# Performance work log

Measured on AMD Instinct MI355X. Metric: run time of the kernel, lower is better.

## Reference

```python
import jax, jax.numpy as jnp
import numpy as np

KSIZE, STRIDE, SCALE = 7, 4, 10.0


def _same_pad_amounts(n, k, s):
    out = -(-n // s)
    pad = max(0, (out - 1) * s + k - n)
    return pad // 2, pad - pad // 2, out


def _conv(x, w, b, stride=1, pad=0):
    y = jax.lax.conv_general_dilated(
        x, w, (stride, stride), [(pad, pad), (pad, pad)],
        dimension_numbers=("NCHW", "OIHW", "NCHW"))
    return y + b[None, :, None, None]


def setup_inputs() -> dict:
    key = jax.random.key(0)
    ks = jax.random.split(key, 10)
    B, Cin, H, W = 2, 64, 256, 256
    Ci = 16                       # inter_channels
    d_in = KSIZE * KSIZE * Ci     # 784 = ksize^2 * inter_channels
    d_out = d_in // 4             # 196
    s = 0.02
    return {
        "b": jax.random.normal(ks[0], (B, Cin, H, W), jnp.float32),
        "g_w": jax.random.normal(ks[1], (Ci, Cin, 3, 3), jnp.float32) * s,
        "g_b": jnp.zeros((Ci,), jnp.float32),
        "theta_w": jax.random.normal(ks[2], (Ci, Cin, 1, 1), jnp.float32) * s,
        "theta_b": jnp.zeros((Ci,), jnp.float32),
        "W_w": jax.random.normal(ks[3], (Cin, Ci, 1, 1), jnp.float32) * s,
        "W_b": jnp.zeros((Cin,), jnp.float32),
        "fc1_w": jax.random.normal(ks[4], (d_out, d_in), jnp.float32) * s,
        "fc1_b": jnp.zeros((d_out,), jnp.float32),
        "fc2_w": jax.random.normal(ks[5], (d_out, d_in), jnp.float32) * s,
        "fc2_b": jnp.zeros((d_out,), jnp.float32),
        "thr_w": jax.random.normal(ks[6], (1, Cin, KSIZE, KSIZE), jnp.float32) * s,
        "thr_b": jnp.zeros((1,), jnp.float32),
        "bias_w": jax.random.normal(ks[7], (1, Cin, KSIZE, KSIZE), jnp.float32) * s,
        "bias_b": jnp.zeros((1,), jnp.float32),
    }


def _forward(b, g_w, g_b, theta_w, theta_b, W_w, W_b, fc1_w, fc1_b,
             fc2_w, fc2_b, thr_w, thr_b, bias_w, bias_b):
    B, Cin, H, W = b.shape
    k, s = KSIZE, STRIDE
    pt, pb, Lh = _same_pad_amounts(H, k, s)
    pl, pr, Lw = _same_pad_amounts(W, k, s)
    L = Lh * Lw
    Ci = g_w.shape[0]

    b1 = _conv(b, g_w, g_b, 1, 1)            # [B,Ci,H,W]
    b2 = _conv(b, theta_w, theta_b, 1, 0)    # [B,Ci,H,W]
    b4 = jnp.pad(b, ((0, 0), (0, 0), (pt, pb), (pl, pr)))
    thr = _conv(b4, thr_w, thr_b, s, 0).reshape(B, L)   # per-patch threshold
    bias = _conv(b4, bias_w, bias_b, s, 0).reshape(B, L)  # per-patch bias

    # patch gather indices on the 'same'-padded grid (torch.Unfold order)
    R = (jnp.arange(Lh) * s)[:, None] + jnp.arange(k)[None, :]   # [Lh,k]
    Cc = (jnp.arange(Lw) * s)[:, None] + jnp.arange(k)[None, :]  # [Lw,k]
    Ri = R[:, None, :, None]                                     # -> [Lh,Lw,k,k]
    Cj = Cc[None, :, None, :]

    def patches(x):  # [B,Ci,H,W] -> [B,L,Ci*k*k], flatten order (C,kh,kw)
        xp = jnp.pad(x, ((0, 0), (0, 0), (pt, pb), (pl, pr)))
        p = xp[:, :, Ri, Cj]                       # [B,Ci,Lh,Lw,k,k]
        return p.transpose(0, 2, 3, 1, 4, 5).reshape(B, L, -1)

    wi = patches(b1)     # stride_1 patches of b1
    xi = wi              # b3 = b1 and stride_1 == stride_2 -> identical patches
    pi = patches(b2)     # stride_2 patches of b2, values to aggregate

    wi_f = jax.nn.relu(jnp.einsum("bld,od->blo", wi, fc1_w) + fc1_b)
    xi_f = jax.nn.relu(jnp.einsum("bld,od->blo", xi, fc2_w) + fc2_b)
    score = jnp.einsum("blo,bmo->blm", wi_f, xi_f)   # [B,L,L] patch similarity

    # threshold-gated sparse attention with learned per-patch thr/bias
    mask = (score >= thr[:, :, None]).astype(score.dtype)
    gated = score * mask + bias[:, :, None]
    attn = jax.nn.softmax(gated * SCALE, axis=-1) * mask
    attn = attn / (attn.sum(-1, keepdims=True) + 1e-8)

    agg = jnp.einsum("blm,bmd->bld", attn, pi)       # [B,L,Ci*k*k]
    p6 = agg.reshape(B, Lh, Lw, Ci, k, k).transpose(0, 3, 1, 2, 4, 5)

    # fold back (sum overlaps), normalize by overlap count, crop padding
    Hp, Wp = H + pt + pb, W + pl + pr
    folded = jnp.zeros((B, Ci, Hp, Wp), score.dtype).at[:, :, Ri, Cj].add(p6)
    cnt = jnp.zeros((Hp, Wp), score.dtype).at[Ri, Cj].add(1.0)
    zi = (folded / cnt)[:, :, pl:pl + H, pt:pt + W]

    return b + _conv(zi, W_w, W_b, 1, 0)


def reference(b, g_w, g_b, theta_w, theta_b, W_w, W_b, fc1_w, fc1_b,
              fc2_w, fc2_b, thr_w, thr_b, bias_w, bias_b):
    return _forward(b, g_w, g_b, theta_w, theta_b, W_w, W_b, fc1_w, fc1_b,
                    fc2_w, fc2_b, thr_w, thr_b, bias_w, bias_b)
```

## Files before the change

kernel.cpp:

```cpp
#include <hip/hip_runtime.h>
#include <math.h>

#define CIN  64
#define CI   16
#define HH   256
#define WWD  256
#define KS   7
#define STR  4
#define LH   64
#define LWD  64
#define LL   4096
#define DIN  784
#define DINP 896
#define DKP  832
#define DOUT 196
#define DOUTP 256
#define NB   2
#define YP   258
#define XP   264

typedef __attribute__((ext_vector_type(8))) short bf16x8;
typedef __attribute__((ext_vector_type(4))) float f32x4;
typedef __attribute__((ext_vector_type(16))) float f32x16;
typedef __attribute__((ext_vector_type(8))) int i32x8;
typedef __attribute__((ext_vector_type(4))) int i32x4;

__device__ __forceinline__ unsigned short f2bf(float x) {
    unsigned int u = __float_as_uint(x);
    unsigned int r = (u + 0x7FFFu + ((u >> 16) & 1u)) >> 16;
    return (unsigned short)r;
}
__device__ __forceinline__ float bf2f(unsigned short h) {
    return __uint_as_float(((unsigned int)h) << 16);
}

__device__ __forceinline__ void stage16(const void* g, void* l) {
#if defined(__has_builtin)
#if __has_builtin(__builtin_amdgcn_global_load_lds)
    __builtin_amdgcn_global_load_lds(
        (const __attribute__((address_space(1))) unsigned int*)g,
        (__attribute__((address_space(3))) unsigned int*)l, 16, 0, 0);
    return;
#endif
#endif
    *(float4*)l = *(const float4*)g;
}

__global__ __launch_bounds__(256) void k_prep_b(const float* __restrict__ b,
                                                unsigned short* __restrict__ bTp) {
    int blk = blockIdx.x;
    int s = blk & 7; int yy = (blk >> 3) % YP; int n = blk / (8 * YP);
    int y = yy - 1;
    for (int xx = threadIdx.x; xx < XP; xx += 256) {
        int x = xx - 4;
        bool v = (y >= 0 && y < 256 && x >= 0 && x < 256);
        unsigned short h[8];
#pragma unroll
        for (int j = 0; j < 8; j++)
            h[j] = v ? f2bf(b[((size_t)(n * 64 + s * 8 + j) * 256 + y) * 256 + x]) : (unsigned short)0;
        *(uint4*)&bTp[((((size_t)n * YP + yy) * 8 + s) * XP + xx) * 8] = *(uint4*)h;
    }
}

__global__ void k_prep_wb(const float* __restrict__ g_w, const float* __restrict__ th_w,
                          unsigned short* __restrict__ wbt) {
    int i = blockIdx.x * 256 + threadIdx.x;
    if (i >= 18432) return;
    int j = i & 7, co = (i >> 3) & 31, q = (i >> 8) & 3, h = (i >> 10) & 1, t = i >> 11;
    int ci = h * 32 + q * 8 + j;
    float v;
    if (co < 16) v = g_w[((size_t)co * 64 + ci) * 9 + t];
    else         v = (t == 4) ? th_w[(size_t)(co - 16) * 64 + ci] : 0.f;
    wbt[i] = f2bf(v);
}

__global__ void k_prep_fc(const float* __restrict__ fc1_w, const float* __restrict__ fc2_w,
                          unsigned short* __restrict__ fcwb) {
    int i = blockIdx.x * 256 + threadIdx.x;
    if (i >= 2 * DOUTP * DKP) return;
    int col = i % DKP; int row = (i / DKP) % DOUTP; int f = i / (DKP * DOUTP);
    float v = 0.f;
    if (row < DOUT && col < DIN) v = (f ? fc2_w : fc1_w)[row * DIN + col];
    fcwb[i] = f2bf(v);
}

__global__ __launch_bounds__(256) void k_convm(
        const unsigned short* __restrict__ bTp, const unsigned short* __restrict__ wbt,
        const float* __restrict__ g_b, const float* __restrict__ th_b,
        unsigned short* __restrict__ bx) {
    __shared__ unsigned short wb[18432];
    __shared__ unsigned short ti[8 * 3 * 68 * 8];
    int tid = threadIdx.x;
#pragma unroll
    for (int i = 0; i < 9; i++) {
        int c = i * 256 + tid;
        stage16(wbt + (size_t)c * 8, &wb[c * 8]);
    }
    int n = blockIdx.x >> 8, y = blockIdx.x & 255;
    int wave = tid >> 6, lane = tid & 63, lr = lane & 15, q = lane >> 4;
    int m0 = wave * 16;
    float bg = g_b[lr], bt = th_b[lr];
    for (int xs = 0; xs < 4; xs++) {
        __syncthreads();
        int x0 = xs * 64;
#pragma unroll
        for (int i = 0; i < 7; i++) {
            int c = i * 256 + tid;
            if (c < 1632) {
                int s = c / 204; int rem = c % 204; int r = rem / 68; int cc = rem % 68;
                const unsigned short* src =
                    bTp + ((((size_t)n * YP + y + r) * 8 + s) * XP + (x0 + 3 + cc)) * 8;
                stage16(src, &ti[c * 8]);
            }
        }
        __syncthreads();
        f32x4 a0 = {bg, bg, bg, bg}, a1 = {bt, bt, bt, bt};
#pragma unroll
        for (int t = 0; t < 9; t++) {
            int dy = t / 3, dx = t % 3;
#pragma unroll
            for (int h = 0; h < 2; h++) {
                int s = h * 4 + q;
                bf16x8 av = *(const bf16x8*)&ti[(((s * 3 + dy) * 68) + m0 + lr + dx) * 8];
                bf16x8 b0 = *(const bf16x8*)&wb[((((t * 2 + h) * 4 + q) * 32) + lr) * 8];
                bf16x8 b1 = *(const bf16x8*)&wb[((((t * 2 + h) * 4 + q) * 32) + 16 + lr) * 8];
                a0 = __builtin_amdgcn_mfma_f32_16x16x32_bf16(av, b0, a0, 0, 0, 0);
                a1 = __builtin_amdgcn_mfma_f32_16x16x32_bf16(av, b1, a1, 0, 0, 0);
            }
        }
        size_t pb = (((size_t)n * 256 + y) * 256 + x0 + m0 + q * 4);
#pragma unroll
        for (int r = 0; r < 4; r++) {
            bx[(pb + r) * 32 + lr]      = f2bf(a0[r]);
            bx[(pb + r) * 32 + 16 + lr] = f2bf(a1[r]);
        }
    }
}

__global__ __launch_bounds__(256) void k_thr(
        const unsigned short* __restrict__ bTp, const float* __restrict__ thr_w,
        const float* __restrict__ thr_b, float* __restrict__ thr) {
    __shared__ float w[64 * 49];
    int tid = threadIdx.x;
    for (int i = tid; i < 64 * 49; i += 256) w[i] = thr_w[i];
    __syncthreads();
    int wid = (blockIdx.x << 2) + (tid >> 6);
    int lane = tid & 63;
    int s = lane >> 3, j = lane & 7;
    int n = wid >> 12, l = wid & 4095;
    int lh = (l >> 6), lw = l & 63;
    const float* wl = w + (s * 8 + j) * 49;
    float acc = 0.f;
#pragma unroll
    for (int dy = 0; dy < 7; dy++) {
        int yy = lh * 4 + dy;
        if (yy >= YP) continue;
        const unsigned short* row = bTp + (((size_t)(n * YP + yy) * 8 + s) * XP) * 8;
#pragma unroll
        for (int dx = 0; dx < 7; dx++) {
            int xx = lw * 4 + dx + 3;
            acc = fmaf(bf2f(row[xx * 8 + j]), wl[dy * 7 + dx], acc);
        }
    }
#pragma unroll
    for (int off = 32; off > 0; off >>= 1) acc += __shfl_down(acc, off, 64);
    if (lane == 0) thr[wid] = acc + thr_b[0];
}

__global__ void k_patchesA(const unsigned short* __restrict__ bx, unsigned short* __restrict__ Pb) {
    size_t e = (size_t)blockIdx.x * 256 + threadIdx.x;
    if (e >= (size_t)NB * LL * DKP) return;
    int d = (int)(e % DKP); size_t r = e / DKP;
    int l = (int)(r & 4095); int n = (int)(r >> 12);
    unsigned short v = 0;
    if (d < DIN) {
        int ci = d / 49; int t = d % 49; int dy = t / 7; int dx = t % 7;
        int y = (l >> 6) * 4 + dy - 1, x = (l & 63) * 4 + dx - 1;
        if (y >= 0 && y < 256 && x >= 0 && x < 256)
            v = bx[(((size_t)n * 256 + y) * 256 + x) * 32 + ci];
    }
    Pb[e] = v;
}

__global__ void k_patchesT(const unsigned short* __restrict__ bx, unsigned char* __restrict__ piT8) {
    size_t e = (size_t)blockIdx.x * 256 + threadIdx.x;
    int l = (int)(e & 4095);
    int d = (int)((e >> 12) % DINP);
    int n = (int)(e / ((size_t)DINP * LL));
    float v = 0.f;
    if (d < DIN) {
        int ci = d / 49; int t = d % 49; int dy = t / 7; int dx = t % 7;
        int y = (l >> 6) * 4 + dy - 1, x = (l & 63) * 4 + dx - 1;
        if (y >= 0 && y < 256 && x >= 0 && x < 256)
            v = bf2f(bx[(((size_t)n * 256 + y) * 256 + x) * 32 + 16 + ci]);
    }
    int p = __builtin_amdgcn_cvt_pk_fp8_f32(v, 0.f, 0, false);
    piT8[e] = (unsigned char)(p & 0xFF);
}

template<int MODE>
__global__ __launch_bounds__(256) void k_gemm_nt(
        const unsigned short* __restrict__ A, const unsigned short* __restrict__ Bt,
        void* __restrict__ C, int lda, int ldb, int ldc, int K,
        size_t sA, size_t sB, size_t sC,
        const float* __restrict__ bias1, const float* __restrict__ bias2) {
    __shared__ unsigned short lA[128 * 64];
    __shared__ unsigned short lB[128 * 64];
    int tid = threadIdx.x;
    int wave = tid >> 6, lane = tid & 63;
    int lr = lane & 15, lq = lane >> 4;
    int wm = (wave >> 1) * 64, wn = (wave & 1) * 64;
    int i0 = blockIdx.x * 128, j0 = blockIdx.y * 128;
    int z = blockIdx.z;
    int az = (MODE == 2) ? (z >> 1) : z;
    int bz = (MODE == 2) ? (z & 1) : z;
    const unsigned short* Ab = A + (size_t)az * sA + (size_t)i0 * lda;
    const unsigned short* Bb = Bt + (size_t)bz * sB + (size_t)j0 * ldb;
    f32x4 acc[4][4] = {};
    for (int k0 = 0; k0 < K; k0 += 64) {
        __syncthreads();
#pragma unroll
        for (int it = 0; it < 4; it++) {
            int c = it * 256 + tid;
            int row = c >> 3, slot = c & 7;
            int col8 = slot ^ (row & 7);
            stage16(Ab + (size_t)row * lda + k0 + col8 * 8, &lA[c * 8]);
        }
#pragma unroll
        for (int it = 0; it < 4; it++) {
            int c = it * 256 + tid;
            int row = c >> 3, slot = c & 7;
            int col8 = slot ^ (row & 7);
            stage16(Bb + (size_t)row * ldb + k0 + col8 * 8, &lB[c * 8]);
        }
        __syncthreads();
#pragma unroll
        for (int ks = 0; ks < 2; ks++) {
            bf16x8 af[4], bfr[4];
#pragma unroll
            for (int t = 0; t < 4; t++) {
                int row = wm + t * 16 + lr;
                int slot = ks * 4 + lq;
                af[t] = *(const bf16x8*)&lA[row * 64 + (slot ^ (row & 7)) * 8];
            }
#pragma unroll
            for (int t = 0; t < 4; t++) {
                int row = wn + t * 16 + lr;
                int slot = ks * 4 + lq;
                bfr[t] = *(const bf16x8*)&lB[row * 64 + (slot ^ (row & 7)) * 8];
            }
#pragma unroll
            for (int mi = 0; mi < 4; mi++)
#pragma unroll
                for (int nj = 0; nj < 4; nj++)
                    acc[mi][nj] = __builtin_amdgcn_mfma_f32_16x16x32_bf16(
                        af[mi], bfr[nj], acc[mi][nj], 0, 0, 0);
        }
    }
    if (MODE == 1) {
        unsigned short* Cb = (unsigned short*)C + (size_t)z * sC;
#pragma unroll
        for (int mi = 0; mi < 4; mi++)
#pragma unroll
            for (int r = 0; r < 4; r++) {
                int row = i0 + wm + mi * 16 + lq * 4 + r;
#pragma unroll
                for (int nj = 0; nj < 4; nj++)
                    Cb[(size_t)row * ldc + j0 + wn + nj * 16 + lr] = f2bf(acc[mi][nj][r]);
            }
    } else {
        const float* biasp = bz ? bias2 : bias1;
        unsigned short* Cb = (unsigned short*)C + (size_t)z * sC;
#pragma unroll
        for (int mi = 0; mi < 4; mi++)
#pragma unroll
            for (int r = 0; r < 4; r++) {
                int row = i0 + wm + mi * 16 + lq * 4 + r;
#pragma unroll
                for (int nj = 0; nj < 4; nj++) {
                    int col = j0 + wn + nj * 16 + lr;
                    float bv = (col < DOUT) ? biasp[col] : 0.f;
                    float v = fmaxf(acc[mi][nj][r] + bv, 0.f);
                    Cb[(size_t)row * ldc + col] = f2bf(v);
                }
            }
    }
}

__global__ __launch_bounds__(256) void k_gemm_mx(
        const unsigned char* __restrict__ A, const unsigned char* __restrict__ Bt,
        unsigned short* __restrict__ C, int lda, int ldb, int ldc, int K,
        size_t sA, size_t sB, size_t sC) {
    __shared__ unsigned char lA[128 * 128];
    __shared__ unsigned char lB[128 * 128];
    int tid = threadIdx.x;
    int wave = tid >> 6, lane = tid & 63;
    int lr = lane & 31, hf = lane >> 5;
    int wm = (wave >> 1) * 64, wn = (wave & 1) * 64;
    int i0 = blockIdx.x * 128, j0 = blockIdx.y * 128;
    int z = blockIdx.z;
    const unsigned char* Ab = A + (size_t)z * sA + (size_t)i0 * lda;
    const unsigned char* Bb = Bt + (size_t)z * sB + (size_t)j0 * ldb;
    f32x16 acc[2][2] = {};
    for (int k0 = 0; k0 < K; k0 += 128) {
        __syncthreads();
#pragma unroll
        for (int it = 0; it < 4; it++) {
            int c = it * 256 + tid;
            int row = c >> 3, slot = c & 7;
            int col16 = slot ^ (row & 7);
            stage16(Ab + (size_t)row * lda + k0 + col16 * 16, &lA[c * 16]);
        }
#pragma unroll
        for (int it = 0; it < 4; it++) {
            int c = it * 256 + tid;
            int row = c >> 3, slot = c & 7;
            int col16 = slot ^ (row & 7);
            stage16(Bb + (size_t)row * ldb + k0 + col16 * 16, &lB[c * 16]);
        }
        __syncthreads();
#pragma unroll
        for (int kk = 0; kk < 2; kk++) {
            i32x8 af[2], bfv[2];
            int c0 = kk * 4 + hf * 2;
#pragma unroll
            for (int t = 0; t < 2; t++) {
                int row = wm + t * 32 + lr;
                i32x4 lo = *(const i32x4*)&lA[row * 128 + ((c0    ) ^ (row & 7)) * 16];
                i32x4 hi = *(const i32x4*)&lA[row * 128 + ((c0 + 1) ^ (row & 7)) * 16];
                af[t][0] = lo[0]; af[t][1] = lo[1]; af[t][2] = lo[2]; af[t][3] = lo[3];
                af[t][4] = hi[0]; af[t][5] = hi[1]; af[t][6] = hi[2]; af[t][7] = hi[3];
            }
#pragma unroll
            for (int t = 0; t < 2; t++) {
                int row = wn + t * 32 + lr;
                i32x4 lo = *(const i32x4*)&lB[row * 128 + ((c0    ) ^ (row & 7)) * 16];
                i32x4 hi = *(const i32x4*)&lB[row * 128 + ((c0 + 1) ^ (row & 7)) * 16];
                bfv[t][0] = lo[0]; bfv[t][1] = lo[1]; bfv[t][2] = lo[2]; bfv[t][3] = lo[3];
                bfv[t][4] = hi[0]; bfv[t][5] = hi[1]; bfv[t][6] = hi[2]; bfv[t][7] = hi[3];
            }
#pragma unroll
            for (int mi = 0; mi < 2; mi++)
#pragma unroll
                for (int nj = 0; nj < 2; nj++)
                    acc[mi][nj] = __builtin_amdgcn_mfma_scale_f32_32x32x64_f8f6f4(
                        af[mi], bfv[nj], acc[mi][nj],
                        0, 0,
                        0, 0x7F7F7F7F,
                        0, 0x7F7F7F7F);
        }
    }
    unsigned short* Cb = C + (size_t)z * sC;
#pragma unroll
    for (int mi = 0; mi < 2; mi++)
#pragma unroll
        for (int nj = 0; nj < 2; nj++)
#pragma unroll
            for (int reg = 0; reg < 16; reg++) {
                int row = i0 + wm + mi * 32 + (reg & 3) + 8 * (reg >> 2) + 4 * hf;
                int col = j0 + wn + nj * 32 + lr;
                Cb[(size_t)row * ldc + col] = f2bf(acc[mi][nj][reg]);
            }
}

__global__ __launch_bounds__(256) void k_softmax(
        const unsigned short* __restrict__ score, const float* __restrict__ thr,
        unsigned char* __restrict__ attn8) {
    __shared__ uint4 srow[512];
    __shared__ float red[256], red2[256];
    int row = blockIdx.x, tid = threadIdx.x;
    const uint4* g4 = (const uint4*)(score + (size_t)row * LL);
    float t = thr[row];
    float mx = 0.f;
#pragma unroll
    for (int c = tid; c < 512; c += 256) {
        uint4 u = g4[c];
        srow[c] = u;
        unsigned int w[4] = {u.x, u.y, u.z, u.w};
#pragma unroll
        for (int qq = 0; qq < 4; qq++) {
            float v0 = __uint_as_float(w[qq] << 16);
            float v1 = __uint_as_float(w[qq] & 0xFFFF0000u);
            if (v0 >= t) mx = fmaxf(mx, v0);
            if (v1 >= t) mx = fmaxf(mx, v1);
        }
    }
    red[tid] = mx; __syncthreads();
    for (int st = 128; st > 0; st >>= 1) {
        if (tid < st) red[tid] = fmaxf(red[tid], red[tid + st]);
        __syncthreads();
    }
    float M = 10.f * fmaxf(red[0], 0.f);
    __syncthreads();
    float s2 = 0.f, n0 = 0.f;
#pragma unroll
    for (int c = tid; c < 512; c += 256) {
        uint4 u = srow[c];
        unsigned int w[4] = {u.x, u.y, u.z, u.w};
#pragma unroll
        for (int qq = 0; qq < 4; qq++) {
            float v0 = __uint_as_float(w[qq] << 16);
            float v1 = __uint_as_float(w[qq] & 0xFFFF0000u);
            if (v0 >= t) s2 += __expf(10.f * v0 - M); else n0 += 1.f;
            if (v1 >= t) s2 += __expf(10.f * v1 - M); else n0 += 1.f;
        }
    }
    red[tid] = s2; red2[tid] = n0; __syncthreads();
    for (int st = 128; st > 0; st >>= 1) {
        if (tid < st) { red[tid] += red[tid + st]; red2[tid] += red2[tid + st]; }
        __syncthreads();
    }
    float S2 = red[0], N0 = red2[0];
    float iD = 1.f / (S2 + 1e-8f * (S2 + N0 * __expf(-M)));
#pragma unroll
    for (int c = tid; c < 512; c += 256) {
        uint4 u = srow[c];
        unsigned int w[4] = {u.x, u.y, u.z, u.w};
        float a[8];
#pragma unroll
        for (int qq = 0; qq < 4; qq++) {
            float v0 = __uint_as_float(w[qq] << 16);
            float v1 = __uint_as_float(w[qq] & 0xFFFF0000u);
            a[2 * qq]     = (v0 >= t) ? __expf(10.f * v0 - M) * iD : 0.f;
            a[2 * qq + 1] = (v1 >= t) ? __expf(10.f * v1 - M) * iD : 0.f;
        }
        int d0 = __builtin_amdgcn_cvt_pk_fp8_f32(a[0], a[1], 0, false);
        d0     = __builtin_amdgcn_cvt_pk_fp8_f32(a[2], a[3], d0, true);
        int d1 = __builtin_amdgcn_cvt_pk_fp8_f32(a[4], a[5], 0, false);
        d1     = __builtin_amdgcn_cvt_pk_fp8_f32(a[6], a[7], d1, true);
        *(uint2*)&attn8[(size_t)row * LL + c * 8] = make_uint2((unsigned)d0, (unsigned)d1);
    }
}

__global__ void k_fold(const unsigned short* __restrict__ aggb, float* __restrict__ zi) {
    int p = blockIdx.x * 256 + threadIdx.x;
    int x = p & 255, y = (p >> 8) & 255, ci = (p >> 16) & 15, n = p >> 20;
    int yp = y + 1, xp = x + 1;
    int lh1 = yp >> 2; if (lh1 > 63) lh1 = 63;
    int lh0 = (yp >= 3) ? ((yp - 3) >> 2) : 0;
    int lw1 = xp >> 2; if (lw1 > 63) lw1 = 63;
    int lw0 = (xp >= 3) ? ((xp - 3) >> 2) : 0;
    const unsigned short* a0 = aggb + (size_t)n * LL * DINP;
    float sum = 0.f;
    for (int lh = lh0; lh <= lh1; lh++) {
        int dy = yp - 4 * lh;
        for (int lw = lw0; lw <= lw1; lw++) {
            int dx = xp - 4 * lw;
            sum += bf2f(a0[(size_t)(lh * 64 + lw) * DINP + ci * 49 + dy * 7 + dx]);
        }
    }
    float cnt = (float)((lh1 - lh0 + 1) * (lw1 - lw0 + 1));
    zi[p] = sum / cnt;
}

__global__ void k_final(const float* __restrict__ zi, const float* __restrict__ b,
                        const float* __restrict__ W_w, const float* __restrict__ W_b,
                        float* __restrict__ out) {
    __shared__ float w[16 * 64];
    int tid = threadIdx.x;
    for (int i = tid; i < 16 * 64; i += 256) {
        int ci = i >> 6; int co = i & 63;
        w[i] = W_w[co * 16 + ci];
    }
    __syncthreads();
    int p = blockIdx.x * 256 + tid;
    int n = p >> 16, yx = p & 65535;
    float acc[64];
#pragma unroll
    for (int co = 0; co < 64; co++) acc[co] = 0.f;
    const float* zn = zi + (size_t)n * 16 * 65536;
#pragma unroll
    for (int ci = 0; ci < 16; ci++) {
        float v = zn[ci * 65536 + yx];
#pragma unroll
        for (int co = 0; co < 64; co++) acc[co] += v * w[ci * 64 + co];
    }
    const float* bn = b + (size_t)n * 64 * 65536;
    float* on = out + (size_t)n * 64 * 65536;
#pragma unroll
    for (int co = 0; co < 64; co++) on[co * 65536 + yx] = bn[co * 65536 + yx] + acc[co] + W_b[co];
}

extern "C" void kernel_launch(void* const* d_in, const int* in_sizes, int n_in,
                              void* d_out, int out_size, void* d_ws, size_t ws_size,
                              hipStream_t stream) {
    const float* b     = (const float*)d_in[0];
    const float* g_w   = (const float*)d_in[1];
    const float* g_b   = (const float*)d_in[2];
    const float* th_w  = (const float*)d_in[3];
    const float* th_b  = (const float*)d_in[4];
    const float* W_w   = (const float*)d_in[5];
    const float* W_b   = (const float*)d_in[6];
    const float* fc1_w = (const float*)d_in[7];
    const float* fc1_b = (const float*)d_in[8];
    const float* fc2_w = (const float*)d_in[9];
    const float* fc2_b = (const float*)d_in[10];
    const float* thr_w = (const float*)d_in[11];
    const float* thr_b = (const float*)d_in[12];
    float* out = (float*)d_out;

    float* ws = (float*)d_ws;
    size_t off = 0;
    auto alloc = [&](size_t nf) { float* p = ws + off; off += (nf + 63) & ~(size_t)63; return p; };
    unsigned short* aggb = (unsigned short*)alloc((size_t)NB * LL * DINP / 2);
    float* zi   = alloc((size_t)NB * CI * HH * WWD);
    unsigned short* bTp  = (unsigned short*)alloc((size_t)NB * YP * 8 * XP * 8 / 2);
    unsigned short* bx   = (unsigned short*)alloc((size_t)NB * HH * WWD * 32 / 2);
    unsigned short* Pb   = (unsigned short*)alloc((size_t)NB * LL * DKP / 2);
    unsigned char*  piT8 = (unsigned char*)alloc((size_t)NB * DINP * LL / 4);
    unsigned short* fcout = (unsigned short*)alloc((size_t)NB * 2 * LL * DOUTP / 2);
    unsigned short* wbt  = (unsigned short*)alloc(18432 / 2);
    unsigned short* fcwb = (unsigned short*)alloc((size_t)2 * DOUTP * DKP / 2);
    float* thr  = alloc((size_t)NB * LL);
    unsigned short* score = (unsigned short*)alloc((size_t)NB * LL * LL / 2);
    unsigned char*  attn8 = (unsigned char*)alloc((size_t)NB * LL * LL / 4);

    k_prep_b<<<dim3(NB * YP * 8), 256, 0, stream>>>(b, bTp);
    k_prep_wb<<<dim3(72), 256, 0, stream>>>(g_w, th_w, wbt);
    k_prep_fc<<<dim3((2 * DOUTP * DKP + 255) / 256), 256, 0, stream>>>(fc1_w, fc2_w, fcwb);
    k_convm<<<dim3(NB * 256), 256, 0, stream>>>(bTp, wbt, g_b, th_b, bx);
    k_thr<<<dim3(2048), 256, 0, stream>>>(bTp, thr_w, thr_b, thr);
    k_patchesA<<<dim3((int)((size_t)NB * LL * DKP / 256)), 256, 0, stream>>>(bx, Pb);
    k_patchesT<<<dim3((int)((size_t)NB * DINP * LL / 256)), 256, 0, stream>>>(bx, piT8);
    k_gemm_nt<2><<<dim3(32, 2, 4), 256, 0, stream>>>(
        Pb, fcwb, (void*)fcout, DKP, DKP, DOUTP, DKP,
        (size_t)LL * DKP, (size_t)DOUTP * DKP, (size_t)LL * DOUTP, fc1_b, fc2_b);
    k_gemm_nt<1><<<dim3(32, 32, NB), 256, 0, stream>>>(
        fcout, fcout + (size_t)LL * DOUTP, (void*)score, DOUTP, DOUTP, LL, DOUTP,
        (size_t)2 * LL * DOUTP, (size_t)2 * LL * DOUTP, (size_t)LL * LL, nullptr, nullptr);
    k_softmax<<<dim3(NB * LL), 256, 0, stream>>>(score, thr, attn8);
    k_gemm_mx<<<dim3(32, DINP / 128, NB), 256, 0, stream>>>(
        attn8, piT8, aggb, LL, LL, DINP, LL,
        (size_t)LL * LL, (size_t)DINP * LL, (size_t)LL * DINP);
    k_fold<<<dim3(8192), 256, 0, stream>>>(aggb, zi);
    k_final<<<dim3(512), 256, 0, stream>>>(zi, b, W_w, W_b, out);
}
```

Before: 335.3 us.

## Split-K the fp8 attention-aggregation GEMM and reduce partials in fold

The fp8 MFMA GEMM computing attn·patches is split into two K halves. This doubles the grid from 448 to 896 blocks so the GPU's CUs are filled more evenly. Each half writes a bf16 partial buffer, and k_fold sums both partials while folding, which doubles that kernel's reads and the workspace. The LDS XOR swizzle is also changed to mix in row>>3, aiming to reduce bank conflicts. Rounding each partial to bf16 before summing adds a small precision loss.

```diff
diff --git a/kernel.cpp b/kernel.cpp
--- a/kernel.cpp
+++ b/kernel.cpp
@@ -18,6 +18,7 @@
 #define NB   2
 #define YP   258
 #define XP   264
+#define SPLITK 2
 
 typedef __attribute__((ext_vector_type(8))) short bf16x8;
 typedef __attribute__((ext_vector_type(4))) float f32x4;
@@ -299,23 +300,25 @@
     int wm = (wave >> 1) * 64, wn = (wave & 1) * 64;
     int i0 = blockIdx.x * 128, j0 = blockIdx.y * 128;
     int z = blockIdx.z;
-    const unsigned char* Ab = A + (size_t)z * sA + (size_t)i0 * lda;
-    const unsigned char* Bb = Bt + (size_t)z * sB + (size_t)j0 * ldb;
+    int nb = z & (NB - 1), sk = z >> 1;
+    const unsigned char* Ab = A + (size_t)nb * sA + (size_t)i0 * lda;
+    const unsigned char* Bb = Bt + (size_t)nb * sB + (size_t)j0 * ldb;
     f32x16 acc[2][2] = {};
-    for (int k0 = 0; k0 < K; k0 += 128) {
+    int kh = K / SPLITK, kbeg = sk * kh;
+    for (int k0 = kbeg; k0 < kbeg + kh; k0 += 128) {
         __syncthreads();
 #pragma unroll
         for (int it = 0; it < 4; it++) {
             int c = it * 256 + tid;
             int row = c >> 3, slot = c & 7;
-            int col16 = slot ^ (row & 7);
+            int col16 = slot ^ ((row ^ (row >> 3)) & 7);
             stage16(Ab + (size_t)row * lda + k0 + col16 * 16, &lA[c * 16]);
         }
 #pragma unroll
         for (int it = 0; it < 4; it++) {
             int c = it * 256 + tid;
             int row = c >> 3, slot = c & 7;
-            int col16 = slot ^ (row & 7);
+            int col16 = slot ^ ((row ^ (row >> 3)) & 7);
             stage16(Bb + (size_t)row * ldb + k0 + col16 * 16, &lB[c * 16]);
         }
         __syncthreads();
@@ -326,16 +329,18 @@
 #pragma unroll
             for (int t = 0; t < 2; t++) {
                 int row = wm + t * 32 + lr;
-                i32x4 lo = *(const i32x4*)&lA[row * 128 + ((c0    ) ^ (row & 7)) * 16];
-                i32x4 hi = *(const i32x4*)&lA[row * 128 + ((c0 + 1) ^ (row & 7)) * 16];
+                int sw = (row ^ (row >> 3)) & 7;
+                i32x4 lo = *(const i32x4*)&lA[row * 128 + ((c0    ) ^ sw) * 16];
+                i32x4 hi = *(const i32x4*)&lA[row * 128 + ((c0 + 1) ^ sw) * 16];
                 af[t][0] = lo[0]; af[t][1] = lo[1]; af[t][2] = lo[2]; af[t][3] = lo[3];
                 af[t][4] = hi[0]; af[t][5] = hi[1]; af[t][6] = hi[2]; af[t][7] = hi[3];
             }
 #pragma unroll
             for (int t = 0; t < 2; t++) {
                 int row = wn + t * 32 + lr;
-                i32x4 lo = *(const i32x4*)&lB[row * 128 + ((c0    ) ^ (row & 7)) * 16];
-                i32x4 hi = *(const i32x4*)&lB[row * 128 + ((c0 + 1) ^ (row & 7)) * 16];
+                int sw = (row ^ (row >> 3)) & 7;
+                i32x4 lo = *(const i32x4*)&lB[row * 128 + ((c0    ) ^ sw) * 16];
+                i32x4 hi = *(const i32x4*)&lB[row * 128 + ((c0 + 1) ^ sw) * 16];
                 bfv[t][0] = lo[0]; bfv[t][1] = lo[1]; bfv[t][2] = lo[2]; bfv[t][3] = lo[3];
                 bfv[t][4] = hi[0]; bfv[t][5] = hi[1]; bfv[t][6] = hi[2]; bfv[t][7] = hi[3];
             }
@@ -441,12 +446,14 @@
     int lw1 = xp >> 2; if (lw1 > 63) lw1 = 63;
     int lw0 = (xp >= 3) ? ((xp - 3) >> 2) : 0;
     const unsigned short* a0 = aggb + (size_t)n * LL * DINP;
+    const unsigned short* a1 = a0 + (size_t)NB * LL * DINP;
     float sum = 0.f;
     for (int lh = lh0; lh <= lh1; lh++) {
         int dy = yp - 4 * lh;
         for (int lw = lw0; lw <= lw1; lw++) {
             int dx = xp - 4 * lw;
-            sum += bf2f(a0[(size_t)(lh * 64 + lw) * DINP + ci * 49 + dy * 7 + dx]);
+            size_t idx = (size_t)(lh * 64 + lw) * DINP + ci * 49 + dy * 7 + dx;
+            sum += bf2f(a0[idx]) + bf2f(a1[idx]);
         }
     }
     float cnt = (float)((lh1 - lh0 + 1) * (lw1 - lw0 + 1));
@@ -502,7 +509,7 @@
     float* ws = (float*)d_ws;
     size_t off = 0;
     auto alloc = [&](size_t nf) { float* p = ws + off; off += (nf + 63) & ~(size_t)63; return p; };
-    unsigned short* aggb = (unsigned short*)alloc((size_t)NB * LL * DINP / 2);
+    unsigned short* aggb = (unsigned short*)alloc((size_t)SPLITK * NB * LL * DINP / 2);
     float* zi   = alloc((size_t)NB * CI * HH * WWD);
     unsigned short* bTp  = (unsigned short*)alloc((size_t)NB * YP * 8 * XP * 8 / 2);
     unsigned short* bx   = (unsigned short*)alloc((size_t)NB * HH * WWD * 32 / 2);
@@ -529,7 +536,7 @@
         fcout, fcout + (size_t)LL * DOUTP, (void*)score, DOUTP, DOUTP, LL, DOUTP,
         (size_t)2 * LL * DOUTP, (size_t)2 * LL * DOUTP, (size_t)LL * LL, nullptr, nullptr);
     k_softmax<<<dim3(NB * LL), 256, 0, stream>>>(score, thr, attn8);
-    k_gemm_mx<<<dim3(32, DINP / 128, NB), 256, 0, stream>>>(
+    k_gemm_mx<<<dim3(32, DINP / 128, NB * SPLITK), 256, 0, stream>>>(
         attn8, piT8, aggb, LL, LL, DINP, LL,
         (size_t)LL * LL, (size_t)DINP * LL, (size_t)LL * DINP);
     k_fold<<<dim3(8192), 256, 0, stream>>>(aggb, zi);
```

New measurement: 338.0 us. Within noise of the previous version (+0.8%).

## Double-buffer LDS staging in MX fp8 GEMM with async prefetch and new swizzle

Applied to the files above, without the earlier changes.

Double-buffers the A/B LDS tiles in the fp8 scaled-MFMA GEMM. Each iteration waits with s_waitcnt vmcnt on the direct-to-LDS loads, then prefetches the tile two steps ahead into the freed buffer, so global loads overlap MFMA work. It also changes the XOR swizzle to mix in row>>3, aiming to cut LDS bank conflicts. LDS use doubles to 64KB per block, which may lower occupancy. Correctness now depends on the hand-written vmcnt(8) count matching the number of outstanding stage16 loads.

```diff
diff --git a/kernel.cpp b/kernel.cpp
--- a/kernel.cpp
+++ b/kernel.cpp
@@ -291,8 +291,8 @@
         const unsigned char* __restrict__ A, const unsigned char* __restrict__ Bt,
         unsigned short* __restrict__ C, int lda, int ldb, int ldc, int K,
         size_t sA, size_t sB, size_t sC) {
-    __shared__ unsigned char lA[128 * 128];
-    __shared__ unsigned char lB[128 * 128];
+    __shared__ unsigned char lA[2][128 * 128];
+    __shared__ unsigned char lB[2][128 * 128];
     int tid = threadIdx.x;
     int wave = tid >> 6, lane = tid & 63;
     int lr = lane & 31, hf = lane >> 5;
@@ -301,43 +301,55 @@
     int z = blockIdx.z;
     const unsigned char* Ab = A + (size_t)z * sA + (size_t)i0 * lda;
     const unsigned char* Bb = Bt + (size_t)z * sB + (size_t)j0 * ldb;
-    f32x16 acc[2][2] = {};
-    for (int k0 = 0; k0 < K; k0 += 128) {
-        __syncthreads();
+
+    auto stageAB = [&](int buf, int k0) {
 #pragma unroll
         for (int it = 0; it < 4; it++) {
             int c = it * 256 + tid;
             int row = c >> 3, slot = c & 7;
-            int col16 = slot ^ (row & 7);
-            stage16(Ab + (size_t)row * lda + k0 + col16 * 16, &lA[c * 16]);
+            int col16 = slot ^ ((row ^ (row >> 3)) & 7);
+            stage16(Ab + (size_t)row * lda + k0 + col16 * 16, &lA[buf][c * 16]);
         }
 #pragma unroll
         for (int it = 0; it < 4; it++) {
             int c = it * 256 + tid;
             int row = c >> 3, slot = c & 7;
-            int col16 = slot ^ (row & 7);
-            stage16(Bb + (size_t)row * ldb + k0 + col16 * 16, &lB[c * 16]);
-        }
-        __syncthreads();
+            int col16 = slot ^ ((row ^ (row >> 3)) & 7);
+            stage16(Bb + (size_t)row * ldb + k0 + col16 * 16, &lB[buf][c * 16]);
+        }
+    };
+
+    f32x16 acc[2][2] = {};
+    int NT = K >> 7;
+    stageAB(0, 0);
+    stageAB(1, 128);
+    for (int t = 0; t < NT; ++t) {
+        int cur = t & 1;
+        if (t + 1 < NT) { asm volatile("s_waitcnt vmcnt(8)" ::: "memory"); }
+        else           { asm volatile("s_waitcnt vmcnt(0)" ::: "memory"); }
+        __builtin_amdgcn_s_barrier();
+        asm volatile("" ::: "memory");
 #pragma unroll
         for (int kk = 0; kk < 2; kk++) {
             i32x8 af[2], bfv[2];
             int c0 = kk * 4 + hf * 2;
 #pragma unroll
-            for (int t = 0; t < 2; t++) {
-                int row = wm + t * 32 + lr;
-                i32x4 lo = *(const i32x4*)&lA[row * 128 + ((c0    ) ^ (row & 7)) * 16];
-                i32x4 hi = *(const i32x4*)&lA[row * 128 + ((c0 + 1) ^ (row & 7)) * 16];
-                af[t][0] = lo[0]; af[t][1] = lo[1]; af[t][2] = lo[2]; af[t][3] = lo[3];
-                af[t][4] = hi[0]; af[t][5] = hi[1]; af[t][6] = hi[2]; af[t][7] = hi[3];
-            }
-#pragma unroll
-            for (int t = 0; t < 2; t++) {
-                int row = wn + t * 32 + lr;
-                i32x4 lo = *(const i32x4*)&lB[row * 128 + ((c0    ) ^ (row & 7)) * 16];
-                i32x4 hi = *(const i32x4*)&lB[row * 128 + ((c0 + 1) ^ (row & 7)) * 16];
-                bfv[t][0] = lo[0]; bfv[t][1] = lo[1]; bfv[t][2] = lo[2]; bfv[t][3] = lo[3];
-                bfv[t][4] = hi[0]; bfv[t][5] = hi[1]; bfv[t][6] = hi[2]; bfv[t][7] = hi[3];
+            for (int t2 = 0; t2 < 2; t2++) {
+                int row = wm + t2 * 32 + lr;
+                int sw = (row ^ (row >> 3)) & 7;
+                i32x4 lo = *(const i32x4*)&lA[cur][row * 128 + ((c0    ) ^ sw) * 16];
+                i32x4 hi = *(const i32x4*)&lA[cur][row * 128 + ((c0 + 1) ^ sw) * 16];
+                af[t2][0] = lo[0]; af[t2][1] = lo[1]; af[t2][2] = lo[2]; af[t2][3] = lo[3];
+                af[t2][4] = hi[0]; af[t2][5] = hi[1]; af[t2][6] = hi[2]; af[t2][7] = hi[3];
+            }
+#pragma unroll
+            for (int t2 = 0; t2 < 2; t2++) {
+                int row = wn + t2 * 32 + lr;
+                int sw = (row ^ (row >> 3)) & 7;
+                i32x4 lo = *(const i32x4*)&lB[cur][row * 128 + ((c0    ) ^ sw) * 16];
+                i32x4 hi = *(const i32x4*)&lB[cur][row * 128 + ((c0 + 1) ^ sw) * 16];
+                bfv[t2][0] = lo[0]; bfv[t2][1] = lo[1]; bfv[t2][2] = lo[2]; bfv[t2][3] = lo[3];
+                bfv[t2][4] = hi[0]; bfv[t2][5] = hi[1]; bfv[t2][6] = hi[2]; bfv[t2][7] = hi[3];
             }
 #pragma unroll
             for (int mi = 0; mi < 2; mi++)
@@ -349,6 +361,9 @@
                         0, 0x7F7F7F7F,
                         0, 0x7F7F7F7F);
         }
+        asm volatile("s_waitcnt lgkmcnt(0)" ::: "memory");
+        __builtin_amdgcn_s_barrier();
+        if (t + 2 < NT) stageAB(cur, (t + 2) << 7);
     }
     unsigned short* Cb = C + (size_t)z * sC;
 #pragma unroll
```

Result: faster. 328.4 us (-2.1%).
